# Performance work log

Measured on AMD Instinct MI355X. Metric: run time of the kernel, lower is better.

## Reference

```python
import jax, jax.numpy as jnp
import numpy as np

N_ITERS = 5
TEMPERATURE = 1.0
EPS = 1e-6


def setup_inputs() -> dict:
    key = jax.random.key(0)
    k1, k2 = jax.random.split(key)
    B, D = 16384, 4096
    x = jax.random.normal(k1, (B, D), dtype=jnp.float32)
    # parameter: eye(dim) + randn(dim, dim), used as log_weight
    log_weight = jnp.eye(D, dtype=jnp.float32) + jax.random.normal(k2, (D, D), dtype=jnp.float32)
    return {"x": x, "log_weight": log_weight}


def reference(x, log_weight):
    # FFT magnitude along feature axis, normalized by per-row max
    xfft = jnp.abs(jnp.fft.fft(x, axis=1))
    xfft = xfft / (jnp.max(xfft, axis=1, keepdims=True) + EPS)
    # Sinkhorn normalization in log space (fixed small iteration count)
    log_P = log_weight / TEMPERATURE
    for _ in range(N_ITERS):
        log_P = log_P - jax.scipy.special.logsumexp(log_P, axis=-1, keepdims=True)
        log_P = log_P - jax.scipy.special.logsumexp(log_P, axis=-2, keepdims=True)
    P = jnp.exp(log_P)
    return (jnp.matmul(xfft, P), P)
```

## Files before the change

kernel.cpp:

```cpp
#include <hip/hip_runtime.h>
#include <hip/hip_bf16.h>
#include <math.h>

#define NROWS 16384
#define DD 4096
#define KK 2048

typedef __attribute__((ext_vector_type(8))) short short8;
typedef __attribute__((ext_vector_type(4))) short short4v;
typedef __attribute__((ext_vector_type(4))) float f32x4;

typedef const __attribute__((address_space(1))) void* gas_cvp;
typedef __attribute__((address_space(3))) void* las_vp;

__device__ __forceinline__ void gload_lds16(const void* g, void* l) {
  __builtin_amdgcn_global_load_lds((gas_cvp)g, (las_vp)l, 16, 0, 0);
}

__device__ __forceinline__ float bf2f(short s) {
  unsigned u = ((unsigned)(unsigned short)s) << 16;
  return __int_as_float((int)u);
}

__device__ __forceinline__ void dft4(float ar, float ai, float br, float bi,
                                     float cr, float ci, float dr, float di,
                                     float& y0r, float& y0i, float& y1r, float& y1i,
                                     float& y2r, float& y2i, float& y3r, float& y3i) {
  float t0r = ar + cr, t0i = ai + ci;
  float t1r = ar - cr, t1i = ai - ci;
  float t2r = br + dr, t2i = bi + di;
  float t3r = br - dr, t3i = bi - di;
  y0r = t0r + t2r; y0i = t0i + t2i;
  y2r = t0r - t2r; y2i = t0i - t2i;
  y1r = t1r + t3i; y1i = t1i - t3r;
  y3r = t1r - t3i; y3i = t1i + t3r;
}

#define C16_1 0.9238795325112867f
#define S16_1 0.3826834323650898f
#define C16_2 0.7071067811865476f

__device__ __forceinline__ void fft16(float* xr, float* xi) {
  const float W16R[10] = {1.f,  C16_1,  C16_2,  S16_1, 0.f, -S16_1, -C16_2, -C16_1, -1.f, -C16_1};
  const float W16I[10] = {0.f, -S16_1, -C16_2, -C16_1, -1.f, -C16_1, -C16_2, -S16_1, 0.f,  S16_1};
  float gr[16], gi[16];
  #pragma unroll
  for (int n2 = 0; n2 < 4; ++n2) {
    dft4(xr[n2], xi[n2], xr[4 + n2], xi[4 + n2], xr[8 + n2], xi[8 + n2], xr[12 + n2], xi[12 + n2],
         gr[0 * 4 + n2], gi[0 * 4 + n2], gr[1 * 4 + n2], gi[1 * 4 + n2],
         gr[2 * 4 + n2], gi[2 * 4 + n2], gr[3 * 4 + n2], gi[3 * 4 + n2]);
  }
  #pragma unroll
  for (int k1 = 1; k1 < 4; ++k1) {
    #pragma unroll
    for (int n2 = 1; n2 < 4; ++n2) {
      const float wr = W16R[k1 * n2], wi = W16I[k1 * n2];
      float a = gr[k1 * 4 + n2], b = gi[k1 * 4 + n2];
      gr[k1 * 4 + n2] = a * wr - b * wi;
      gi[k1 * 4 + n2] = a * wi + b * wr;
    }
  }
  #pragma unroll
  for (int k1 = 0; k1 < 4; ++k1) {
    dft4(gr[k1 * 4 + 0], gi[k1 * 4 + 0], gr[k1 * 4 + 1], gi[k1 * 4 + 1],
         gr[k1 * 4 + 2], gi[k1 * 4 + 2], gr[k1 * 4 + 3], gi[k1 * 4 + 3],
         xr[k1 + 0], xi[k1 + 0], xr[k1 + 4], xi[k1 + 4],
         xr[k1 + 8], xi[k1 + 8], xr[k1 + 12], xi[k1 + 12]);
  }
}

#define TWIDDLE16(xr, xi, w1r, w1i)                                               \
  {                                                                               \
    float pr[16], pi[16];                                                         \
    pr[1] = (w1r); pi[1] = (w1i);                                                 \
    _Pragma("unroll") for (int _z = 0; _z < 1; ++_z) {                            \
      pr[2] = pr[1]*pr[1] - pi[1]*pi[1];  pi[2] = 2.f*pr[1]*pi[1];                \
      pr[4] = pr[2]*pr[2] - pi[2]*pi[2];  pi[4] = 2.f*pr[2]*pi[2];                \
      pr[8] = pr[4]*pr[4] - pi[4]*pi[4];  pi[8] = 2.f*pr[4]*pi[4];                \
      pr[3] = pr[1]*pr[2] - pi[1]*pi[2];  pi[3] = pr[1]*pi[2] + pi[1]*pr[2];      \
      pr[5] = pr[1]*pr[4] - pi[1]*pi[4];  pi[5] = pr[1]*pi[4] + pi[1]*pr[4];      \
      pr[6] = pr[2]*pr[4] - pi[2]*pi[4];  pi[6] = pr[2]*pi[4] + pi[2]*pr[4];      \
      pr[7] = pr[3]*pr[4] - pi[3]*pi[4];  pi[7] = pr[3]*pi[4] + pi[3]*pr[4];      \
      pr[9] = pr[1]*pr[8] - pi[1]*pi[8];  pi[9] = pr[1]*pi[8] + pi[1]*pr[8];      \
      pr[10] = pr[2]*pr[8] - pi[2]*pi[8]; pi[10] = pr[2]*pi[8] + pi[2]*pr[8];     \
      pr[11] = pr[3]*pr[8] - pi[3]*pi[8]; pi[11] = pr[3]*pi[8] + pi[3]*pr[8];     \
      pr[12] = pr[4]*pr[8] - pi[4]*pi[8]; pi[12] = pr[4]*pi[8] + pi[4]*pr[8];     \
      pr[13] = pr[5]*pr[8] - pi[5]*pi[8]; pi[13] = pr[5]*pi[8] + pi[5]*pr[8];     \
      pr[14] = pr[6]*pr[8] - pi[6]*pi[8]; pi[14] = pr[6]*pi[8] + pi[6]*pr[8];     \
      pr[15] = pr[7]*pr[8] - pi[7]*pi[8]; pi[15] = pr[7]*pi[8] + pi[7]*pr[8];     \
    }                                                                             \
    _Pragma("unroll") for (int k = 1; k < 16; ++k) {                              \
      float aa = (xr)[k], bb = (xi)[k];                                           \
      (xr)[k] = aa * pr[k] - bb * pi[k];                                          \
      (xi)[k] = aa * pi[k] + bb * pr[k];                                          \
    }                                                                             \
  }

__global__ __launch_bounds__(256) void k_fftmag(const float* __restrict__ x,
                                                __hip_bfloat16* __restrict__ Af,
                                                float* __restrict__ a0f) {
  __shared__ float lsh[8704];
  float* lre = lsh;
  float* lim = lsh + 4352;
  const int t = threadIdx.x;
  const size_t row0 = (size_t)blockIdx.x * 2;
  const float* __restrict__ xa = x + row0 * DD;
  const float* __restrict__ xb = xa + DD;

  float xr[16], xi[16];

  #pragma unroll
  for (int n1 = 0; n1 < 16; ++n1) {
    xr[n1] = xa[n1 * 256 + t];
    xi[n1] = xb[n1 * 256 + t];
  }
  fft16(xr, xi);
  {
    float w1r, w1i;
    __sincosf(-6.283185307179586f * (float)t / 4096.0f, &w1i, &w1r);
    TWIDDLE16(xr, xi, w1r, w1i);
  }
  #pragma unroll
  for (int k1 = 0; k1 < 16; ++k1) {
    lre[k1 * 272 + t] = xr[k1];
    lim[k1 * 272 + t] = xi[k1];
  }
  __syncthreads();

  const int k1 = t >> 4;
  const int m2 = t & 15;
  #pragma unroll
  for (int m1 = 0; m1 < 16; ++m1) {
    xr[m1] = lre[k1 * 272 + m1 * 16 + m2];
    xi[m1] = lim[k1 * 272 + m1 * 16 + m2];
  }
  fft16(xr, xi);
  {
    float w1r, w1i;
    __sincosf(-6.283185307179586f * (float)m2 / 256.0f, &w1i, &w1r);
    TWIDDLE16(xr, xi, w1r, w1i);
  }
  __syncthreads();
  #pragma unroll
  for (int j1 = 0; j1 < 16; ++j1) {
    lre[j1 * 256 + k1 * 16 + (m2 ^ j1)] = xr[j1];
    lim[j1 * 256 + k1 * 16 + (m2 ^ j1)] = xi[j1];
  }
  __syncthreads();

  const int j1 = t & 15;
  #pragma unroll
  for (int mm = 0; mm < 16; ++mm) {
    xr[mm] = lre[j1 * 256 + k1 * 16 + (mm ^ j1)];
    xi[mm] = lim[j1 * 256 + k1 * 16 + (mm ^ j1)];
  }
  fft16(xr, xi);

  __syncthreads();
  #pragma unroll
  for (int j2 = 0; j2 < 16; ++j2) {
    const int c = k1 + 16 * j1 + 256 * j2;
    const int ad = c + (c >> 4);
    lre[ad] = xr[j2];
    lim[ad] = xi[j2];
  }
  __syncthreads();

  float ma[8], mb[8];
  float mxa = 0.0f, mxb = 0.0f;
  #pragma unroll
  for (int e = 0; e < 8; ++e) {
    const int c = 8 * t + 1 + e;
    const int m = 4096 - c;
    const float zr = lre[c + (c >> 4)], zi = lim[c + (c >> 4)];
    const float wr_ = lre[m + (m >> 4)], wi_ = lim[m + (m >> 4)];
    const float ar_ = 0.5f * (zr + wr_), ai_ = 0.5f * (zi - wi_);
    const float br_ = 0.5f * (zi + wi_), bi_ = 0.5f * (wr_ - zr);
    ma[e] = sqrtf(ar_ * ar_ + ai_ * ai_);
    mb[e] = sqrtf(br_ * br_ + bi_ * bi_);
    mxa = fmaxf(mxa, ma[e]);
    mxb = fmaxf(mxb, mb[e]);
  }
  float m0a = 0.f, m0b = 0.f;
  if (t == 0) {
    m0a = fabsf(lre[0]);
    m0b = fabsf(lim[0]);
    mxa = fmaxf(mxa, m0a);
    mxb = fmaxf(mxb, m0b);
  }
  #pragma unroll
  for (int off = 32; off > 0; off >>= 1) {
    mxa = fmaxf(mxa, __shfl_xor(mxa, off));
    mxb = fmaxf(mxb, __shfl_xor(mxb, off));
  }
  __shared__ float wmaxa[4], wmaxb[4];
  if ((t & 63) == 0) { wmaxa[t >> 6] = mxa; wmaxb[t >> 6] = mxb; }
  __syncthreads();
  mxa = fmaxf(fmaxf(wmaxa[0], wmaxa[1]), fmaxf(wmaxa[2], wmaxa[3]));
  mxb = fmaxf(fmaxf(wmaxb[0], wmaxb[1]), fmaxf(wmaxb[2], wmaxb[3]));
  const float inva = 1.0f / (mxa + 1e-6f);
  const float invb = 1.0f / (mxb + 1e-6f);

  short8 oa, ob;
  #pragma unroll
  for (int e = 0; e < 8; ++e) {
    __hip_bfloat16 v;
    v = __float2bfloat16(ma[e] * inva); oa[e] = *(const short*)&v;
    v = __float2bfloat16(mb[e] * invb); ob[e] = *(const short*)&v;
  }
  *(short8*)&Af[row0 * KK + 8 * t] = oa;
  *(short8*)&Af[(row0 + 1) * KK + 8 * t] = ob;
  if (t == 0) {
    a0f[row0] = m0a * inva;
    a0f[row0 + 1] = m0b * invb;
  }
}

__global__ __launch_bounds__(256) void k_exp(const float* __restrict__ w,
                                             __hip_bfloat16* __restrict__ E) {
  const f32x4* __restrict__ w4 = (const f32x4*)w;
  int idx = blockIdx.x * 256 + threadIdx.x;
  #pragma unroll
  for (int k = 0; k < 8; ++k) {
    f32x4 v = w4[idx];
    short4v o;
    #pragma unroll
    for (int q = 0; q < 4; ++q) {
      __hip_bfloat16 b = __float2bfloat16(__expf(v[q]));
      o[q] = *(const short*)&b;
    }
    *(short4v*)&E[(size_t)idx * 4] = o;
    idx += 524288;
  }
}

__global__ __launch_bounds__(256) void k_row_mv(const __hip_bfloat16* __restrict__ E,
                                                const float* __restrict__ u,
                                                float* __restrict__ rinv) {
  const int i = blockIdx.x;
  const int t = threadIdx.x;
  const short8* __restrict__ e8 = (const short8*)(E + (size_t)i * DD);
  const f32x4* __restrict__ u4 = (const f32x4*)u;
  float s = 0.f;
  #pragma unroll
  for (int g = 0; g < 2; ++g) {
    const int idx = t + g * 256;
    short8 ev = e8[idx];
    if (u4) {
      f32x4 ua = u4[idx * 2], ub = u4[idx * 2 + 1];
      s += bf2f(ev[0]) * ua[0] + bf2f(ev[1]) * ua[1] +
           bf2f(ev[2]) * ua[2] + bf2f(ev[3]) * ua[3] +
           bf2f(ev[4]) * ub[0] + bf2f(ev[5]) * ub[1] +
           bf2f(ev[6]) * ub[2] + bf2f(ev[7]) * ub[3];
    } else {
      s += (bf2f(ev[0]) + bf2f(ev[1])) + (bf2f(ev[2]) + bf2f(ev[3])) +
           (bf2f(ev[4]) + bf2f(ev[5])) + (bf2f(ev[6]) + bf2f(ev[7]));
    }
  }
  #pragma unroll
  for (int off = 32; off > 0; off >>= 1) s += __shfl_xor(s, off);
  __shared__ float ss[4];
  if ((t & 63) == 0) ss[t >> 6] = s;
  __syncthreads();
  if (t == 0) rinv[i] = 1.0f / ((ss[0] + ss[1]) + (ss[2] + ss[3]));
}

__global__ __launch_bounds__(256) void k_col_mv(const __hip_bfloat16* __restrict__ E,
                                                const float* __restrict__ rinv,
                                                float* __restrict__ ps) {
  const int j8 = blockIdx.x * 256 + threadIdx.x;
  const int i0 = blockIdx.y * 32;
  float s0 = 0.f, s1 = 0.f, s2 = 0.f, s3 = 0.f;
  float s4 = 0.f, s5 = 0.f, s6 = 0.f, s7 = 0.f;
  const short8* __restrict__ e8 = (const short8*)E;
  #pragma unroll 4
  for (int ii = 0; ii < 32; ++ii) {
    const int i = i0 + ii;
    const float rv = rinv[i];
    short8 ev = e8[(size_t)i * (DD / 8) + j8];
    s0 += bf2f(ev[0]) * rv;
    s1 += bf2f(ev[1]) * rv;
    s2 += bf2f(ev[2]) * rv;
    s3 += bf2f(ev[3]) * rv;
    s4 += bf2f(ev[4]) * rv;
    s5 += bf2f(ev[5]) * rv;
    s6 += bf2f(ev[6]) * rv;
    s7 += bf2f(ev[7]) * rv;
  }
  f32x4 a; a[0] = s0; a[1] = s1; a[2] = s2; a[3] = s3;
  f32x4 b; b[0] = s4; b[1] = s5; b[2] = s6; b[3] = s7;
  ((f32x4*)ps)[(size_t)blockIdx.y * (DD / 4) + j8 * 2] = a;
  ((f32x4*)ps)[(size_t)blockIdx.y * (DD / 4) + j8 * 2 + 1] = b;
}

__global__ __launch_bounds__(256) void k_col_final(const float* __restrict__ ps,
                                                   float* __restrict__ uinv) {
  const int j = blockIdx.x * 256 + threadIdx.x;
  float s = 0.0f;
  #pragma unroll 4
  for (int k = 0; k < 128; ++k) {
    s += ps[(size_t)k * DD + j];
  }
  uinv[j] = 1.0f / s;
}

__global__ __launch_bounds__(256) void k_pfinal(const float* __restrict__ w,
                                                const float* __restrict__ rinv,
                                                const float* __restrict__ uinv,
                                                float* __restrict__ P) {
  const f32x4* __restrict__ w4 = (const f32x4*)w;
  const f32x4* __restrict__ u4 = (const f32x4*)uinv;
  f32x4* __restrict__ P4 = (f32x4*)P;
  int idx = blockIdx.x * 256 + threadIdx.x;
  #pragma unroll
  for (int k = 0; k < 8; ++k) {
    f32x4 wv = w4[idx];
    f32x4 uv = u4[idx & 1023];
    const float rv = rinv[idx >> 10];
    f32x4 pv;
    #pragma unroll
    for (int q = 0; q < 4; ++q) pv[q] = __expf(wv[q]) * rv * uv[q];
    P4[idx] = pv;
    idx += 524288;
  }
}

__global__ __launch_bounds__(256) void k_btf(const float* __restrict__ P,
                                             __hip_bfloat16* __restrict__ BtF) {
  __shared__ __hip_bfloat16 tile[64][68];
  const int t = threadIdx.x;
  const int tx = t & 63;
  const int ty = t >> 6;
  const int k0 = blockIdx.x * 64;
  const int j0 = blockIdx.y * 64;
  #pragma unroll
  for (int p = 0; p < 16; ++p) {
    const int kk = p * 4 + ty;
    const int k = k0 + kk;
    float s;
    if (k == 2047) {
      s = P[(size_t)2048 * DD + j0 + tx];
    } else {
      s = P[(size_t)(k + 1) * DD + j0 + tx] + P[(size_t)(4095 - k) * DD + j0 + tx];
    }
    tile[kk][tx] = __float2bfloat16(s);
  }
  __syncthreads();
  const int txg = t & 15;
  const int ty2 = t >> 4;
  #pragma unroll
  for (int p = 0; p < 4; ++p) {
    const int rr = p * 16 + ty2;
    short4v o;
    #pragma unroll
    for (int q = 0; q < 4; ++q)
      o[q] = *(const short*)&tile[txg * 4 + q][rr];
    *(short4v*)&BtF[(size_t)(j0 + rr) * KK + k0 + txg * 4] = o;
  }
}

__global__ __launch_bounds__(512, 2) void k_gemm256(const __hip_bfloat16* __restrict__ A,
                                                    const __hip_bfloat16* __restrict__ Bt,
                                                    const float* __restrict__ a0f,
                                                    const float* __restrict__ p0,
                                                    float* __restrict__ C) {
  __shared__ alignas(16) char lds[131072];
  const int tid = threadIdx.x;
  const int lane = tid & 63;
  const int wid = tid >> 6;
  const int wm = wid >> 2;
  const int wn = wid & 3;

  const int bid = blockIdx.x;
  const int swz = (bid & 7) * 32 + (bid >> 3);
  const int ntile = swz & 15;
  const int mgroup = swz >> 4;
  const size_t brow = (size_t)ntile * 256;

  const int srow = tid >> 2;
  const int scolb = ((tid & 3) << 4) ^ (((tid >> 5) & 1) << 5);
  const __hip_bfloat16* gB = Bt + (brow + srow) * (size_t)KK + (scolb >> 1);
  const __hip_bfloat16* gAcur =
      A + ((size_t)mgroup * 4 * 256 + srow) * (size_t)KK + (scolb >> 1);

#define STG(gbase, regionoff, kt, ks) do {                                        \
    const __hip_bfloat16* _g = (gbase) + (kt) * 64 + (ks) * 32;                   \
    char* _l = lds + (regionoff) + (((kt) & 1) * 32768) + (ks) * 16384 + tid * 16;\
    gload_lds16(_g, _l);                                                          \
    gload_lds16(_g + (size_t)128 * KK, _l + 8192);                                \
  } while (0)
#define STG_A(kt, ks) STG(gAcur, 0, kt, ks)
#define STG_B(kt, ks) STG(gB, 65536, kt, ks)

  const int lr = lane & 15;
  const int rcol = ((lane >> 4) << 4) ^ (((lr >> 3) & 1) << 5);
  const int rbA = (wm * 128 + lr) * 64 + rcol;
  const int rbB = (wn * 64 + lr) * 64 + rcol;

#define LD8(off) (*reinterpret_cast<const short8*>(lds + (off)))
#define RD_B(BUF, KS)                                                   \
  { b[0] = LD8(65536 + (BUF) * 32768 + (KS) * 16384 + rbB + 0);         \
    b[1] = LD8(65536 + (BUF) * 32768 + (KS) * 16384 + rbB + 1024);      \
    b[2] = LD8(65536 + (BUF) * 32768 + (KS) * 16384 + rbB + 2048);      \
    b[3] = LD8(65536 + (BUF) * 32768 + (KS) * 16384 + rbB + 3072); }
#define RD_A4(BUF, KS, MH, DST)                                                   \
  { a[(DST) + 0] = LD8((BUF) * 32768 + (KS) * 16384 + rbA + (MH) * 4096 + 0);     \
    a[(DST) + 1] = LD8((BUF) * 32768 + (KS) * 16384 + rbA + (MH) * 4096 + 1024);  \
    a[(DST) + 2] = LD8((BUF) * 32768 + (KS) * 16384 + rbA + (MH) * 4096 + 2048);  \
    a[(DST) + 3] = LD8((BUF) * 32768 + (KS) * 16384 + rbA + (MH) * 4096 + 3072); }

#define BAR __builtin_amdgcn_s_barrier()
#define LGKM0 asm volatile("s_waitcnt lgkmcnt(0)" ::: "memory")
#define VM6 asm volatile("s_waitcnt vmcnt(6)" ::: "memory")
#define VM0 asm volatile("s_waitcnt vmcnt(0)" ::: "memory")

#define MFMA16(MH)                                                                \
  __builtin_amdgcn_s_setprio(1);                                                  \
  { _Pragma("unroll") for (int i = 0; i < 4; ++i) {                               \
      _Pragma("unroll") for (int n = 0; n < 4; ++n) {                             \
        acc[(MH) * 4 + i][n] = __builtin_amdgcn_mfma_f32_16x16x32_bf16(           \
            a[(MH) * 4 + i], b[n], acc[(MH) * 4 + i][n], 0, 0, 0); } } }          \
  __builtin_amdgcn_s_setprio(0);

#define KTILE(BUF, TN1, TN2)            \
  RD_B(BUF, 0); RD_A4(BUF, 0, 0, 0);    \
  STG_B(TN1, 1);                        \
  BAR; LGKM0; MFMA16(0); BAR;           \
  RD_A4(BUF, 0, 1, 4);                  \
  STG_B(TN2, 0);                        \
  BAR; LGKM0; MFMA16(1); BAR;           \
  RD_B(BUF, 1); RD_A4(BUF, 1, 0, 0);    \
  STG_A(TN2, 0);                        \
  BAR; LGKM0; MFMA16(0); BAR;           \
  RD_A4(BUF, 1, 1, 4);                  \
  BAR; LGKM0;                           \
  STG_A(TN2, 1); VM6;                   \
  MFMA16(1); BAR;

#define KTILE_F0                        \
  RD_B(0, 0); RD_A4(0, 0, 0, 0);        \
  STG_B(31, 1);                         \
  BAR; LGKM0; MFMA16(0); BAR;           \
  RD_A4(0, 0, 1, 4);                    \
  BAR; LGKM0; MFMA16(1); BAR;           \
  RD_B(0, 1); RD_A4(0, 1, 0, 0);        \
  BAR; LGKM0; MFMA16(0); BAR;           \
  RD_A4(0, 1, 1, 4);                    \
  BAR; LGKM0; VM0; MFMA16(1); BAR;

#define KTILE_F1                        \
  RD_B(1, 0); RD_A4(1, 0, 0, 0);        \
  BAR; LGKM0; MFMA16(0); BAR;           \
  RD_A4(1, 0, 1, 4);                    \
  BAR; LGKM0; MFMA16(1); BAR;           \
  RD_B(1, 1); RD_A4(1, 1, 0, 0);        \
  BAR; LGKM0; MFMA16(0); BAR;           \
  RD_A4(1, 1, 1, 4);                    \
  BAR; LGKM0; MFMA16(1); BAR;

  f32x4 acc[8][4];
  short8 a[8], b[4];

  STG_B(0, 0); STG_A(0, 0); STG_A(0, 1); STG_B(0, 1);
  STG_B(1, 0); STG_A(1, 0); STG_A(1, 1);
  VM6;
  BAR;

  for (int st = 0; st < 4; ++st) {
    #pragma unroll
    for (int i = 0; i < 8; ++i)
      #pragma unroll
      for (int n = 0; n < 4; ++n) {
        acc[i][n][0] = 0.f; acc[i][n][1] = 0.f; acc[i][n][2] = 0.f; acc[i][n][3] = 0.f;
      }

    for (int kt = 0; kt < 30; kt += 2) {
      KTILE(0, kt + 1, kt + 2);
      KTILE(1, kt + 2, kt + 3);
    }
    KTILE_F0;
    KTILE_F1;

    const size_t arow = (size_t)(mgroup * 4 + st) * 256;

    if (st < 3) {
      const __hip_bfloat16* gAn = gAcur + (size_t)256 * KK;
      STG(gB, 65536, 0, 0); STG(gAn, 0, 0, 0); STG(gAn, 0, 0, 1); STG(gB, 65536, 0, 1);
      STG(gB, 65536, 1, 0); STG(gAn, 0, 1, 0); STG(gAn, 0, 1, 1);
      gAcur = gAn;
    }

    const int orow = (lane >> 4) * 4;
    const int ocol = lane & 15;
    float p0n[4];
    #pragma unroll
    for (int n = 0; n < 4; ++n)
      p0n[n] = p0[brow + (size_t)wn * 64 + n * 16 + ocol];
    #pragma unroll
    for (int mh = 0; mh < 2; ++mh) {
      #pragma unroll
      for (int i = 0; i < 4; ++i) {
        const size_t rbase = arow + (size_t)wm * 128 + mh * 64 + i * 16 + orow;
        const f32x4 av = *(const f32x4*)&a0f[rbase];
        #pragma unroll
        for (int n = 0; n < 4; ++n) {
          const size_t ccol = brow + (size_t)wn * 64 + n * 16 + ocol;
          #pragma unroll
          for (int jj = 0; jj < 4; ++jj) {
            C[(rbase + jj) * DD + ccol] = acc[mh * 4 + i][n][jj] + av[jj] * p0n[n];
          }
        }
      }
    }

    if (st < 3) { VM6; BAR; }
  }
#undef STG
#undef STG_A
#undef STG_B
#undef LD8
#undef RD_B
#undef RD_A4
#undef BAR
#undef LGKM0
#undef VM6
#undef VM0
#undef MFMA16
#undef KTILE
#undef KTILE_F0
#undef KTILE_F1
}

extern "C" void kernel_launch(void* const* d_in, const int* in_sizes, int n_in,
                              void* d_out, int out_size, void* d_ws, size_t ws_size,
                              hipStream_t stream) {
  const float* x = (const float*)d_in[0];
  const float* w = (const float*)d_in[1];
  float* outMM = (float*)d_out;
  float* outP = (float*)d_out + (size_t)NROWS * DD;

  char* ws = (char*)d_ws;
  __hip_bfloat16* Af = (__hip_bfloat16*)ws;
  __hip_bfloat16* Breg = (__hip_bfloat16*)(ws + (size_t)NROWS * KK * 2);
  __hip_bfloat16* E = Breg;
  __hip_bfloat16* BtF = Breg;
  float* rinv = (float*)(ws + (size_t)NROWS * KK * 2 + (size_t)DD * DD * 2);
  float* uinv = rinv + DD;
  float* a0f = uinv + DD;
  float* ps = a0f + NROWS;

  k_fftmag<<<NROWS / 2, 256, 0, stream>>>(x, Af, a0f);
  k_exp<<<2048, 256, 0, stream>>>(w, E);
  for (int it = 0; it < 5; ++it) {
    k_row_mv<<<DD, 256, 0, stream>>>(E, it == 0 ? (const float*)nullptr : uinv, rinv);
    k_col_mv<<<dim3(2, 128), 256, 0, stream>>>(E, rinv, ps);
    k_col_final<<<16, 256, 0, stream>>>(ps, uinv);
  }
  k_pfinal<<<2048, 256, 0, stream>>>(w, rinv, uinv, outP);
  k_btf<<<dim3(KK / 64, DD / 64), 256, 0, stream>>>(outP, BtF);
  k_gemm256<<<256, 512, 0, stream>>>(Af, BtF, a0f, outP, outMM);
}
```

Baseline: 531.3 us.

## Fuse final P computation into BtF fold kernel and move GEMM barrier earlier

Removes the separate k_pfinal pass and computes each P element (exp(w)*rinv*uinv) inside the fold/transpose kernel, which writes P and builds the bf16 folded B operand in the same pass. Row 0 is handled by a tiny separate kernel. This saves a full read of the 64MB P matrix. Separately, the GEMM's wait and barrier after prefetch are moved before the epilogue stores instead of after, which changes how prefetch overlaps with output writes.

Result: no change. 521.4 us (-1.9%).

```diff
diff --git a/kernel.cpp b/kernel.cpp
--- a/kernel.cpp
+++ b/kernel.cpp
@@ -304,28 +304,18 @@
   uinv[j] = 1.0f / s;
 }
 
-__global__ __launch_bounds__(256) void k_pfinal(const float* __restrict__ w,
-                                                const float* __restrict__ rinv,
-                                                const float* __restrict__ uinv,
-                                                float* __restrict__ P) {
-  const f32x4* __restrict__ w4 = (const f32x4*)w;
-  const f32x4* __restrict__ u4 = (const f32x4*)uinv;
-  f32x4* __restrict__ P4 = (f32x4*)P;
-  int idx = blockIdx.x * 256 + threadIdx.x;
-  #pragma unroll
-  for (int k = 0; k < 8; ++k) {
-    f32x4 wv = w4[idx];
-    f32x4 uv = u4[idx & 1023];
-    const float rv = rinv[idx >> 10];
-    f32x4 pv;
-    #pragma unroll
-    for (int q = 0; q < 4; ++q) pv[q] = __expf(wv[q]) * rv * uv[q];
-    P4[idx] = pv;
-    idx += 524288;
-  }
-}
-
-__global__ __launch_bounds__(256) void k_btf(const float* __restrict__ P,
+__global__ __launch_bounds__(256) void k_p0(const float* __restrict__ w,
+                                            const float* __restrict__ rinv,
+                                            const float* __restrict__ uinv,
+                                            float* __restrict__ P) {
+  const int j = blockIdx.x * 256 + threadIdx.x;
+  P[j] = __expf(w[j]) * rinv[0] * uinv[j];
+}
+
+__global__ __launch_bounds__(256) void k_pfb(const float* __restrict__ w,
+                                             const float* __restrict__ rinv,
+                                             const float* __restrict__ uinv,
+                                             float* __restrict__ P,
                                              __hip_bfloat16* __restrict__ BtF) {
   __shared__ __hip_bfloat16 tile[64][68];
   const int t = threadIdx.x;
@@ -333,15 +323,20 @@
   const int ty = t >> 6;
   const int k0 = blockIdx.x * 64;
   const int j0 = blockIdx.y * 64;
+  const float uv = uinv[j0 + tx];
   #pragma unroll
   for (int p = 0; p < 16; ++p) {
     const int kk = p * 4 + ty;
     const int k = k0 + kk;
-    float s;
-    if (k == 2047) {
-      s = P[(size_t)2048 * DD + j0 + tx];
-    } else {
-      s = P[(size_t)(k + 1) * DD + j0 + tx] + P[(size_t)(4095 - k) * DD + j0 + tx];
+    const int r1 = k + 1;
+    const int r2 = 4095 - k;
+    float p1 = __expf(w[(size_t)r1 * DD + j0 + tx]) * rinv[r1] * uv;
+    P[(size_t)r1 * DD + j0 + tx] = p1;
+    float s = p1;
+    if (r2 != r1) {
+      float p2 = __expf(w[(size_t)r2 * DD + j0 + tx]) * rinv[r2] * uv;
+      P[(size_t)r2 * DD + j0 + tx] = p2;
+      s += p2;
     }
     tile[kk][tx] = __float2bfloat16(s);
   }
@@ -488,6 +483,8 @@
       STG(gB, 65536, 0, 0); STG(gAn, 0, 0, 0); STG(gAn, 0, 0, 1); STG(gB, 65536, 0, 1);
       STG(gB, 65536, 1, 0); STG(gAn, 0, 1, 0); STG(gAn, 0, 1, 1);
       gAcur = gAn;
+      VM6;
+      BAR;
     }
 
     const int orow = (lane >> 4) * 4;
@@ -512,8 +509,6 @@
         }
       }
     }
-
-    if (st < 3) { VM6; BAR; }
   }
 #undef STG
 #undef STG_A
@@ -556,7 +551,7 @@
     k_col_mv<<<dim3(2, 128), 256, 0, stream>>>(E, rinv, ps);
     k_col_final<<<16, 256, 0, stream>>>(ps, uinv);
   }
-  k_pfinal<<<2048, 256, 0, stream>>>(w, rinv, uinv, outP);
-  k_btf<<<dim3(KK / 64, DD / 64), 256, 0, stream>>>(outP, BtF);
+  k_p0<<<16, 256, 0, stream>>>(w, rinv, uinv, outP);
+  k_pfb<<<dim3(KK / 64, DD / 64), 256, 0, stream>>>(w, rinv, uinv, outP, BtF);
   k_gemm256<<<256, 512, 0, stream>>>(Af, BtF, a0f, outP, outMM);
 }
```
